# Performance work log

Hardware: AMD Instinct MI355X
Metric: run time of the kernel (lower is better)

Reference implementation:

```python
import jax, jax.numpy as jnp
import numpy as np

N = 100000   # nodes
E = 1600000  # edges
F = 128      # num_features
H = 128      # embedding_size
C = 10       # num_classes
G = 64       # graphs in batch


def setup_inputs() -> dict:
    key = jax.random.key(0)
    ks = jax.random.split(key, 10)
    x = jax.random.normal(ks[0], (N, F), jnp.float32)
    edge_index = jax.random.randint(ks[1], (2, E), 0, N)
    batch_index = jnp.sort(jax.random.randint(ks[2], (N,), 0, G))
    glorot = lambda k, shape: jax.random.normal(k, shape, jnp.float32) / np.float32(np.sqrt(shape[0]))
    return {
        "x": x, "edge_index": edge_index, "batch_index": batch_index,
        "W0": glorot(ks[3], (F, H)), "b0": jnp.zeros((H,), jnp.float32),
        "W1": glorot(ks[4], (H, H)), "b1": jnp.zeros((H,), jnp.float32),
        "W2": glorot(ks[5], (H, H)), "b2": jnp.zeros((H,), jnp.float32),
        "W3": glorot(ks[6], (H, H)), "b3": jnp.zeros((H,), jnp.float32),
        "Wout": glorot(ks[7], (2 * H, C)), "bout": jnp.zeros((C,), jnp.float32),
    }


def gcn_conv(x, W, b, src, dst):
    """PyG GCNConv: self-loops + symmetric D^-1/2 (A+I) D^-1/2 normalization."""
    n = x.shape[0]
    # degree with self-loop: deg[i] = 1 + in-degree(i)
    deg = 1.0 + jax.ops.segment_sum(jnp.ones(dst.shape[0], x.dtype), dst, num_segments=n)
    dinv = jax.lax.rsqrt(deg)
    h = x @ W  # [N, H]
    norm = (dinv[src] * dinv[dst])[:, None]  # [E, 1]
    agg = jax.ops.segment_sum(h[src] * norm, dst, num_segments=n)  # scatter-add over edges
    agg = agg + h * (1.0 / deg)[:, None]  # self-loop contribution dinv[i]^2 * h[i]
    return agg + b


def reference(x, edge_index, batch_index, W0, b0, W1, b1, W2, b2, W3, b3, Wout, bout):
    src, dst = edge_index[0], edge_index[1]
    h = jnp.tanh(gcn_conv(x, W0, b0, src, dst))
    h = jnp.tanh(gcn_conv(h, W1, b1, src, dst))
    h = jnp.tanh(gcn_conv(h, W2, b2, src, dst))
    h = jnp.tanh(gcn_conv(h, W3, b3, src, dst))
    # global max pool + global mean pool over batch_index
    gmax = jax.ops.segment_max(h, batch_index, num_segments=G)
    cnt = jax.ops.segment_sum(jnp.ones((h.shape[0],), h.dtype), batch_index, num_segments=G)
    gmean = jax.ops.segment_sum(h, batch_index, num_segments=G) / jnp.maximum(cnt, 1.0)[:, None]
    pooled = jnp.concatenate([gmax, gmean], axis=1)  # [G, 2H]
    out = pooled @ Wout + bout  # [G, C]
    return out, pooled
```

## Files before the change

### kernel.cpp

```cpp
#include <hip/hip_runtime.h>
#include <hip/hip_fp16.h>
#include <cmath>

typedef __attribute__((ext_vector_type(8))) short short8;
typedef __attribute__((ext_vector_type(8))) unsigned short ushort8;
typedef __attribute__((ext_vector_type(4))) float f32x4;

struct h8 { __half2 a, b, c, d; };

__device__ __forceinline__ unsigned pk_bf16(float a, float b) {
  unsigned r;
  asm("v_cvt_pk_bf16_f32 %0, %1, %2" : "=v"(r) : "v"(a), "v"(b));
  return r;
}

__device__ __forceinline__ float fast_tanh(float x) {
  float e2 = __expf(2.0f * x);
  return 1.0f - 2.0f * __builtin_amdgcn_rcpf(e2 + 1.0f);
}


__global__ __launch_bounds__(256) void count_k(const int* __restrict__ dst,
                                               int* __restrict__ cnt,
                                               int* __restrict__ epos, int E) {
  int e = blockIdx.x * 256 + threadIdx.x;
  if (e < E) epos[e] = atomicAdd(&cnt[dst[e]], 1);
}

__global__ __launch_bounds__(512) void scan_a(const int* __restrict__ cnt,
                                              int* __restrict__ rs,
                                              int* __restrict__ bsum,
                                              float* __restrict__ dinv,
                                              float* __restrict__ dinv2, int n) {
  __shared__ int s[512];
  int tid = threadIdx.x;
  int gid = blockIdx.x * 512 + tid;
  int v = (gid < n) ? cnt[gid] : 0;
  if (gid < n) {
    float deg = 1.0f + (float)v;
    dinv[gid] = rsqrtf(deg);
    dinv2[gid] = __builtin_amdgcn_rcpf(deg);
  }
  s[tid] = v;
  __syncthreads();
  for (int off = 1; off < 512; off <<= 1) {
    int t = (tid >= off) ? s[tid - off] : 0;
    __syncthreads();
    s[tid] += t;
    __syncthreads();
  }
  if (gid < n) rs[gid] = s[tid] - v;
  if (tid == 511) bsum[blockIdx.x] = s[511];
}

__global__ __launch_bounds__(256) void scan_b(const int* __restrict__ bsum,
                                              int* __restrict__ boff, int nb,
                                              const int* __restrict__ batch,
                                              int* __restrict__ gstart, int n,
                                              int G) {
  __shared__ int s[256];
  int tid = threadIdx.x;
  int v = (tid < nb) ? bsum[tid] : 0;
  s[tid] = v;
  __syncthreads();
  for (int off = 1; off < 256; off <<= 1) {
    int t = (tid >= off) ? s[tid - off] : 0;
    __syncthreads();
    s[tid] += t;
    __syncthreads();
  }
  if (tid < nb) boff[tid] = s[tid] - v;
  if (tid <= G) {
    int lo = 0, hi = n;
    while (lo < hi) {
      int mid = (lo + hi) >> 1;
      if (batch[mid] < tid) lo = mid + 1;
      else hi = mid;
    }
    gstart[tid] = lo;
  }
}

__global__ __launch_bounds__(512) void scan_c(const int* __restrict__ boff,
                                              int* __restrict__ rs, int n, int E) {
  int gid = blockIdx.x * 512 + threadIdx.x;
  if (gid < n) rs[gid] += boff[blockIdx.x];
  if (gid == 0) rs[n] = E;
}

__global__ __launch_bounds__(256) void fill_k(const int* __restrict__ src,
                                              const int* __restrict__ dst,
                                              const int* __restrict__ rs,
                                              const int* __restrict__ epos,
                                              const float* __restrict__ dinv,
                                              int2* __restrict__ edata, int E) {
  int e = blockIdx.x * 256 + threadIdx.x;
  if (e >= E) return;
  int s = src[e], d = dst[e];
  int pos = rs[d] + epos[e];
  int2 ed;
  ed.x = s;
  ed.y = __float_as_int(dinv[s] * dinv[d]);
  edata[pos] = ed;
}


__global__ __launch_bounds__(256) void wconv_all(const float* __restrict__ W0,
                                                 const float* __restrict__ W1,
                                                 const float* __restrict__ W2,
                                                 const float* __restrict__ W3,
                                                 unsigned short* __restrict__ WtHi,
                                                 unsigned short* __restrict__ WtLo) {
  int l = blockIdx.y;
  const float* W = (l == 0) ? W0 : (l == 1) ? W1 : (l == 2) ? W2 : W3;
  int idx = blockIdx.x * 256 + threadIdx.x;
  if (idx >= 8192) return;
  int n = idx & 127, k = (idx >> 7) * 2;
  float w0 = W[k * 128 + n], w1 = W[(k + 1) * 128 + n];
  unsigned h01 = pk_bf16(w0, w1);
  float hf0 = __uint_as_float(h01 << 16);
  float hf1 = __uint_as_float(h01 & 0xFFFF0000u);
  unsigned l01 = pk_bf16(w0 - hf0, w1 - hf1);
  *(unsigned*)&WtHi[l * 16384 + n * 128 + k] = h01;
  *(unsigned*)&WtLo[l * 16384 + n * 128 + k] = l01;
}


#define LDK 136

__global__ __launch_bounds__(256) void gemm_mfma(const float* __restrict__ A,
                                                 const unsigned short* __restrict__ WtHi,
                                                 const unsigned short* __restrict__ WtLo,
                                                 __half* __restrict__ O, int M) {
  __shared__ unsigned short sHi[128 * LDK];
  __shared__ unsigned short sLo[128 * LDK];
  int tid = threadIdx.x;
#pragma unroll
  for (int i = 0; i < 8; ++i) {
    int c = tid + i * 256;
    int n = c >> 4;
    int off = (c & 15) * 8;
    *(ushort8*)&sHi[n * LDK + off] = *(const ushort8*)&WtHi[c * 8];
    *(ushort8*)&sLo[n * LDK + off] = *(const ushort8*)&WtLo[c * 8];
  }
  __syncthreads();

  int wv = tid >> 6, lane = tid & 63;
  int r0 = blockIdx.x * 128 + wv * 32;
  int lrow = lane & 15, lk = (lane >> 4) * 8;

  f32x4 acc[2][8] = {};
#pragma unroll
  for (int kk = 0; kk < 4; ++kk) {
    int k0 = kk * 32 + lk;
    short8 ahi[2], alo[2];
#pragma unroll
    for (int fr = 0; fr < 2; ++fr) {
      int row = r0 + fr * 16 + lrow;
      row = row < M ? row : M - 1;
      const float* ap = &A[(size_t)row * 128 + k0];
      float4 a0 = *(const float4*)ap;
      float4 a1 = *(const float4*)(ap + 4);
      union { short8 v; unsigned u32[4]; } h_, l_;
#define SPLIT2(slot, x, y)                              \
      {                                                 \
        unsigned hh = pk_bf16((x), (y));                \
        h_.u32[slot] = hh;                              \
        float hf0 = __uint_as_float(hh << 16);          \
        float hf1 = __uint_as_float(hh & 0xFFFF0000u);  \
        l_.u32[slot] = pk_bf16((x) - hf0, (y) - hf1);   \
      }
      SPLIT2(0, a0.x, a0.y)
      SPLIT2(1, a0.z, a0.w)
      SPLIT2(2, a1.x, a1.y)
      SPLIT2(3, a1.z, a1.w)
#undef SPLIT2
      ahi[fr] = h_.v;
      alo[fr] = l_.v;
    }
#pragma unroll
    for (int c = 0; c < 8; ++c) {
      int bidx = (c * 16 + lrow) * LDK + k0;
      short8 bhi = *(const short8*)&sHi[bidx];
      short8 blo = *(const short8*)&sLo[bidx];
#pragma unroll
      for (int fr = 0; fr < 2; ++fr) {
        acc[fr][c] = __builtin_amdgcn_mfma_f32_16x16x32_bf16(ahi[fr], bhi, acc[fr][c], 0, 0, 0);
        acc[fr][c] = __builtin_amdgcn_mfma_f32_16x16x32_bf16(ahi[fr], blo, acc[fr][c], 0, 0, 0);
        acc[fr][c] = __builtin_amdgcn_mfma_f32_16x16x32_bf16(alo[fr], bhi, acc[fr][c], 0, 0, 0);
      }
    }
  }
#pragma unroll
  for (int fr = 0; fr < 2; ++fr) {
#pragma unroll
    for (int c = 0; c < 8; ++c) {
#pragma unroll
      for (int r = 0; r < 4; ++r) {
        int row = r0 + fr * 16 + (lane >> 4) * 4 + r;
        if (row < M)
          O[(size_t)row * 128 + c * 16 + (lane & 15)] = __float2half(acc[fr][c][r]);
      }
    }
  }
}

__global__ __launch_bounds__(256) void gemm_fast(const unsigned short* __restrict__ AHi,
                                                 const unsigned short* __restrict__ ALo,
                                                 const unsigned short* __restrict__ WtHi,
                                                 const unsigned short* __restrict__ WtLo,
                                                 __half* __restrict__ O, int M) {
  __shared__ unsigned short sHi[128 * LDK];
  __shared__ unsigned short sLo[128 * LDK];
  int tid = threadIdx.x;
#pragma unroll
  for (int i = 0; i < 8; ++i) {
    int c = tid + i * 256;
    int n = c >> 4;
    int off = (c & 15) * 8;
    *(ushort8*)&sHi[n * LDK + off] = *(const ushort8*)&WtHi[c * 8];
    *(ushort8*)&sLo[n * LDK + off] = *(const ushort8*)&WtLo[c * 8];
  }
  __syncthreads();

  int wv = tid >> 6, lane = tid & 63;
  int r0 = blockIdx.x * 128 + wv * 32;
  int lrow = lane & 15, lk = (lane >> 4) * 8;

  f32x4 acc[2][8] = {};
#pragma unroll
  for (int kk = 0; kk < 4; ++kk) {
    int k0 = kk * 32 + lk;
    short8 ahi[2], alo[2];
#pragma unroll
    for (int fr = 0; fr < 2; ++fr) {
      int row = r0 + fr * 16 + lrow;
      row = row < M ? row : M - 1;
      ahi[fr] = *(const short8*)&AHi[(size_t)row * 128 + k0];
      alo[fr] = *(const short8*)&ALo[(size_t)row * 128 + k0];
    }
#pragma unroll
    for (int c = 0; c < 8; ++c) {
      int bidx = (c * 16 + lrow) * LDK + k0;
      short8 bhi = *(const short8*)&sHi[bidx];
      short8 blo = *(const short8*)&sLo[bidx];
#pragma unroll
      for (int fr = 0; fr < 2; ++fr) {
        acc[fr][c] = __builtin_amdgcn_mfma_f32_16x16x32_bf16(ahi[fr], bhi, acc[fr][c], 0, 0, 0);
        acc[fr][c] = __builtin_amdgcn_mfma_f32_16x16x32_bf16(ahi[fr], blo, acc[fr][c], 0, 0, 0);
        acc[fr][c] = __builtin_amdgcn_mfma_f32_16x16x32_bf16(alo[fr], bhi, acc[fr][c], 0, 0, 0);
      }
    }
  }
#pragma unroll
  for (int fr = 0; fr < 2; ++fr) {
#pragma unroll
    for (int c = 0; c < 8; ++c) {
#pragma unroll
      for (int r = 0; r < 4; ++r) {
        int row = r0 + fr * 16 + (lane >> 4) * 4 + r;
        if (row < M)
          O[(size_t)row * 128 + c * 16 + (lane & 15)] = __float2half(acc[fr][c][r]);
      }
    }
  }
}


__global__ __launch_bounds__(256) void gather_k(const __half* __restrict__ h,
                                                const int* __restrict__ rs,
                                                const int2* __restrict__ edata,
                                                const float* __restrict__ dinv2,
                                                const float* __restrict__ bias,
                                                unsigned* __restrict__ OHi,
                                                unsigned* __restrict__ OLo, int N) {
  int wid = (int)((blockIdx.x * (size_t)blockDim.x + threadIdx.x) >> 6);
  if (wid >= N) return;
  int lane = threadIdx.x & 63;
  int grp = lane >> 4;
  int li = lane & 15;
  int s = rs[wid], e = rs[wid + 1];
  const h8* hrow = (const h8*)h;

  float ac[8] = {};
  int n16 = (e - s) >> 4;
  int base = s + grp;
  for (int it = 0; it < n16; ++it, base += 16) {
    int2 e0 = edata[base], e1 = edata[base + 4], e2 = edata[base + 8],
         e3 = edata[base + 12];
    float w0 = __int_as_float(e0.y), w1 = __int_as_float(e1.y),
          w2 = __int_as_float(e2.y), w3 = __int_as_float(e3.y);
    h8 v0 = hrow[(size_t)e0.x * 16 + li];
    h8 v1 = hrow[(size_t)e1.x * 16 + li];
    h8 v2 = hrow[(size_t)e2.x * 16 + li];
    h8 v3 = hrow[(size_t)e3.x * 16 + li];
#define ACC(V, W)                                    \
    {                                                \
      float2 f0 = __half22float2((V).a);             \
      float2 f1 = __half22float2((V).b);             \
      float2 f2 = __half22float2((V).c);             \
      float2 f3 = __half22float2((V).d);             \
      ac[0] += (W) * f0.x; ac[1] += (W) * f0.y;      \
      ac[2] += (W) * f1.x; ac[3] += (W) * f1.y;      \
      ac[4] += (W) * f2.x; ac[5] += (W) * f2.y;      \
      ac[6] += (W) * f3.x; ac[7] += (W) * f3.y;      \
    }
    ACC(v0, w0) ACC(v1, w1) ACC(v2, w2) ACC(v3, w3)
  }
  for (int idx = base; idx < e; idx += 4) {
    int2 ed = edata[idx];
    float w = __int_as_float(ed.y);
    h8 v = hrow[(size_t)ed.x * 16 + li];
    ACC(v, w)
  }
#undef ACC
#pragma unroll
  for (int j = 0; j < 8; ++j) {
    ac[j] += __shfl_xor(ac[j], 16);
    ac[j] += __shfl_xor(ac[j], 32);
  }

  float a0 = grp == 0 ? ac[0] : grp == 1 ? ac[2] : grp == 2 ? ac[4] : ac[6];
  float a1 = grp == 0 ? ac[1] : grp == 1 ? ac[3] : grp == 2 ? ac[5] : ac[7];

  float d2 = dinv2[wid];
  h8 sv = hrow[(size_t)wid * 16 + li];
  __half2 svh = grp == 0 ? sv.a : grp == 1 ? sv.b : grp == 2 ? sv.c : sv.d;
  float2 sj = __half22float2(svh);
  float2 bj = *(const float2*)&bias[li * 8 + 2 * grp];
  float o0 = fast_tanh(a0 + sj.x * d2 + bj.x);
  float o1 = fast_tanh(a1 + sj.y * d2 + bj.y);

  unsigned hp = pk_bf16(o0, o1);
  float r0f = __uint_as_float(hp << 16);
  float r1f = __uint_as_float(hp & 0xFFFF0000u);
  unsigned lp = pk_bf16(o0 - r0f, o1 - r1f);
  unsigned idx = (unsigned)wid * 64 + li * 4 + grp;
  OHi[idx] = hp;
  OLo[idx] = lp;
}


#define CH 16

__global__ __launch_bounds__(128) void pool_partial(const unsigned short* __restrict__ Hi,
                                                    const unsigned short* __restrict__ Lo,
                                                    const int* __restrict__ gstart,
                                                    float* __restrict__ pmax,
                                                    float* __restrict__ psum) {
  int g = blockIdx.x, c = blockIdx.y, f = threadIdx.x;
  int s = gstart[g], e = gstart[g + 1];
  long long len = e - s;
  int cs = s + (int)(len * c / CH);
  int ce = s + (int)(len * (c + 1) / CH);
  float m = -INFINITY, sum = 0.f;
  for (int n = cs; n < ce; ++n) {
    unsigned hv = Hi[(size_t)n * 128 + f];
    unsigned lv = Lo[(size_t)n * 128 + f];
    float v = __uint_as_float(hv << 16) + __uint_as_float(lv << 16);
    m = fmaxf(m, v);
    sum += v;
  }
  pmax[((size_t)g * CH + c) * 128 + f] = m;
  psum[((size_t)g * CH + c) * 128 + f] = sum;
}

__global__ __launch_bounds__(128) void pool_head(const float* __restrict__ pmax,
                                                 const float* __restrict__ psum,
                                                 const int* __restrict__ gstart,
                                                 const float* __restrict__ Wout,
                                                 const float* __restrict__ bout,
                                                 float* __restrict__ out, int G) {
  __shared__ float pl[256];
  int g = blockIdx.x, f = threadIdx.x;
  float m = -INFINITY, s = 0.f;
  for (int c = 0; c < CH; ++c) {
    m = fmaxf(m, pmax[((size_t)g * CH + c) * 128 + f]);
    s += psum[((size_t)g * CH + c) * 128 + f];
  }
  int cnt = gstart[g + 1] - gstart[g];
  float mean = s / fmaxf((float)cnt, 1.0f);
  float* pooled = out + (size_t)G * 10;
  pooled[(size_t)g * 256 + f] = m;
  pooled[(size_t)g * 256 + 128 + f] = mean;
  pl[f] = m;
  pl[128 + f] = mean;
  __syncthreads();
  if (f < 10) {
    float acc = bout[f];
    for (int k = 0; k < 256; ++k) acc += pl[k] * Wout[k * 10 + f];
    out[(size_t)g * 10 + f] = acc;
  }
}


extern "C" void kernel_launch(void* const* d_in, const int* in_sizes, int n_in,
                              void* d_out, int out_size, void* d_ws, size_t ws_size,
                              hipStream_t stream) {
  const float* x = (const float*)d_in[0];
  const int* ei = (const int*)d_in[1];
  const int* batch = (const int*)d_in[2];
  const float* W[4] = {(const float*)d_in[3], (const float*)d_in[5],
                       (const float*)d_in[7], (const float*)d_in[9]};
  const float* Bz[4] = {(const float*)d_in[4], (const float*)d_in[6],
                        (const float*)d_in[8], (const float*)d_in[10]};
  const float* Wout = (const float*)d_in[11];
  const float* bout = (const float*)d_in[12];
  const int N = in_sizes[0] / 128;
  const int E = in_sizes[1] / 2;
  const int G = 64;
  const int* srcp = ei;
  const int* dstp = ei + E;
  float* out = (float*)d_out;

  char* wsb = (char*)d_ws;
  size_t off = 0;
  auto alloc = [&](size_t bytes) -> void* {
    void* p = wsb + off;
    off = (off + bytes + 255) & ~(size_t)255;
    return p;
  };
  __half* bufA = (__half*)alloc((size_t)N * 128 * 2);
  unsigned* OHi = (unsigned*)alloc((size_t)N * 64 * 4);
  unsigned* OLo = (unsigned*)alloc((size_t)N * 64 * 4);
  int* cnt = (int*)alloc((size_t)N * 4);
  int* epos = (int*)alloc((size_t)E * 4);
  float* dinv = (float*)alloc((size_t)N * 4);
  float* dinv2 = (float*)alloc((size_t)N * 4);
  int* rs = (int*)alloc((size_t)(N + 1) * 4);
  int2* edata = (int2*)alloc((size_t)E * 8);
  int* bsum = (int*)alloc(4096);
  int* boff = (int*)alloc(4096);
  int* gstart = (int*)alloc(4096);
  float* pmax = (float*)alloc((size_t)G * CH * 128 * 4);
  float* psum = (float*)alloc((size_t)G * CH * 128 * 4);
  unsigned short* WtHi = (unsigned short*)alloc(4 * 16384 * 2);
  unsigned short* WtLo = (unsigned short*)alloc(4 * 16384 * 2);
  if (off > ws_size) return;

  hipMemsetAsync(cnt, 0, (size_t)N * 4, stream);

  count_k<<<(E + 255) / 256, 256, 0, stream>>>(dstp, cnt, epos, E);
  int nsb = (N + 511) / 512;
  scan_a<<<nsb, 512, 0, stream>>>(cnt, rs, bsum, dinv, dinv2, N);
  scan_b<<<1, 256, 0, stream>>>(bsum, boff, nsb, batch, gstart, N, G);
  scan_c<<<nsb, 512, 0, stream>>>(boff, rs, N, E);
  fill_k<<<(E + 255) / 256, 256, 0, stream>>>(srcp, dstp, rs, epos, dinv, edata, E);
  wconv_all<<<dim3(32, 4), 256, 0, stream>>>(W[0], W[1], W[2], W[3], WtHi, WtLo);

  for (int l = 0; l < 4; ++l) {
    if (l == 0)
      gemm_mfma<<<(N + 127) / 128, 256, 0, stream>>>(x, WtHi, WtLo, bufA, N);
    else
      gemm_fast<<<(N + 127) / 128, 256, 0, stream>>>((const unsigned short*)OHi,
                                                     (const unsigned short*)OLo,
                                                     WtHi + l * 16384,
                                                     WtLo + l * 16384, bufA, N);
    gather_k<<<((size_t)N * 64 + 255) / 256, 256, 0, stream>>>(bufA, rs, edata,
                                                               dinv2, Bz[l], OHi,
                                                               OLo, N);
  }

  pool_partial<<<dim3(G, CH), 128, 0, stream>>>((const unsigned short*)OHi,
                                                (const unsigned short*)OLo, gstart,
                                                pmax, psum);
  pool_head<<<G, 128, 0, stream>>>(pmax, psum, gstart, Wout, bout, out, G);
}
```

Before: 537.2 us.

## Store intermediate activations in fp16 and use split-fp16 weight MFMA for layers 1-3

The gather kernel now writes intermediate-layer activations as a single fp16 array instead of bf16 hi/lo pairs, which halves the bytes written and read between layers. Layers 1-3 use a new fp16 MFMA GEMM in which the weights are split into an fp16 high part and a residual scaled by 1024. This cuts the MFMA count from three to two per tile. The gather inner loop uses v_fma_mix_f32 to multiply fp16 values directly without explicit conversion. The cost is lower activation precision (fp16 in place of about 16-bit-mantissa bf16 pairs), and only the final layer keeps the hi/lo output for pooling.

```diff
diff --git a/kernel.cpp b/kernel.cpp
--- a/kernel.cpp
+++ b/kernel.cpp
@@ -4,9 +4,8 @@
 
 typedef __attribute__((ext_vector_type(8))) short short8;
 typedef __attribute__((ext_vector_type(8))) unsigned short ushort8;
+typedef __attribute__((ext_vector_type(8))) _Float16 f16x8;
 typedef __attribute__((ext_vector_type(4))) float f32x4;
-
-struct h8 { __half2 a, b, c, d; };
 
 __device__ __forceinline__ unsigned pk_bf16(float a, float b) {
   unsigned r;
@@ -18,6 +17,11 @@
   float e2 = __expf(2.0f * x);
   return 1.0f - 2.0f * __builtin_amdgcn_rcpf(e2 + 1.0f);
 }
+
+#define FM_LO(A, U, W) \
+  asm("v_fma_mix_f32 %0, %1, %2, %0 op_sel_hi:[1,0,0]" : "+v"(A) : "v"(U), "v"(W))
+#define FM_HI(A, U, W) \
+  asm("v_fma_mix_f32 %0, %1, %2, %0 op_sel:[1,0,0] op_sel_hi:[1,0,0]" : "+v"(A) : "v"(U), "v"(W))
 
 
 __global__ __launch_bounds__(256) void count_k(const int* __restrict__ dst,
@@ -109,20 +113,31 @@
                                                  const float* __restrict__ W1,
                                                  const float* __restrict__ W2,
                                                  const float* __restrict__ W3,
-                                                 unsigned short* __restrict__ WtHi,
-                                                 unsigned short* __restrict__ WtLo) {
+                                                 unsigned short* __restrict__ Wt0Hi,
+                                                 unsigned short* __restrict__ Wt0Lo,
+                                                 unsigned short* __restrict__ WfHi,
+                                                 unsigned short* __restrict__ WfLo) {
   int l = blockIdx.y;
   const float* W = (l == 0) ? W0 : (l == 1) ? W1 : (l == 2) ? W2 : W3;
   int idx = blockIdx.x * 256 + threadIdx.x;
   if (idx >= 8192) return;
   int n = idx & 127, k = (idx >> 7) * 2;
   float w0 = W[k * 128 + n], w1 = W[(k + 1) * 128 + n];
-  unsigned h01 = pk_bf16(w0, w1);
-  float hf0 = __uint_as_float(h01 << 16);
-  float hf1 = __uint_as_float(h01 & 0xFFFF0000u);
-  unsigned l01 = pk_bf16(w0 - hf0, w1 - hf1);
-  *(unsigned*)&WtHi[l * 16384 + n * 128 + k] = h01;
-  *(unsigned*)&WtLo[l * 16384 + n * 128 + k] = l01;
+  if (l == 0) {
+    unsigned h01 = pk_bf16(w0, w1);
+    float hf0 = __uint_as_float(h01 << 16);
+    float hf1 = __uint_as_float(h01 & 0xFFFF0000u);
+    unsigned l01 = pk_bf16(w0 - hf0, w1 - hf1);
+    *(unsigned*)&Wt0Hi[n * 128 + k] = h01;
+    *(unsigned*)&Wt0Lo[n * 128 + k] = l01;
+  } else {
+    __half2 hh = __float22half2_rn(make_float2(w0, w1));
+    float r0 = __low2float(hh), r1 = __high2float(hh);
+    __half2 ll = __float22half2_rn(make_float2((w0 - r0) * 1024.0f,
+                                               (w1 - r1) * 1024.0f));
+    *(__half2*)&WfHi[(l - 1) * 16384 + n * 128 + k] = hh;
+    *(__half2*)&WfLo[(l - 1) * 16384 + n * 128 + k] = ll;
+  }
 }
 
 
@@ -205,11 +220,11 @@
   }
 }
 
-__global__ __launch_bounds__(256) void gemm_fast(const unsigned short* __restrict__ AHi,
-                                                 const unsigned short* __restrict__ ALo,
-                                                 const unsigned short* __restrict__ WtHi,
-                                                 const unsigned short* __restrict__ WtLo,
-                                                 __half* __restrict__ O, int M) {
+
+__global__ __launch_bounds__(256) void gemm_f16(const __half* __restrict__ Hf,
+                                                const unsigned short* __restrict__ Whi,
+                                                const unsigned short* __restrict__ Wlo,
+                                                __half* __restrict__ O, int M) {
   __shared__ unsigned short sHi[128 * LDK];
   __shared__ unsigned short sLo[128 * LDK];
   int tid = threadIdx.x;
@@ -218,8 +233,8 @@
     int c = tid + i * 256;
     int n = c >> 4;
     int off = (c & 15) * 8;
-    *(ushort8*)&sHi[n * LDK + off] = *(const ushort8*)&WtHi[c * 8];
-    *(ushort8*)&sLo[n * LDK + off] = *(const ushort8*)&WtLo[c * 8];
+    *(ushort8*)&sHi[n * LDK + off] = *(const ushort8*)&Whi[c * 8];
+    *(ushort8*)&sLo[n * LDK + off] = *(const ushort8*)&Wlo[c * 8];
   }
   __syncthreads();
 
@@ -228,30 +243,30 @@
   int lrow = lane & 15, lk = (lane >> 4) * 8;
 
   f32x4 acc[2][8] = {};
+  f32x4 accL[2][8] = {};
 #pragma unroll
   for (int kk = 0; kk < 4; ++kk) {
     int k0 = kk * 32 + lk;
-    short8 ahi[2], alo[2];
+    f16x8 a[2];
 #pragma unroll
     for (int fr = 0; fr < 2; ++fr) {
       int row = r0 + fr * 16 + lrow;
       row = row < M ? row : M - 1;
-      ahi[fr] = *(const short8*)&AHi[(size_t)row * 128 + k0];
-      alo[fr] = *(const short8*)&ALo[(size_t)row * 128 + k0];
+      a[fr] = *(const f16x8*)&Hf[(size_t)row * 128 + k0];
     }
 #pragma unroll
     for (int c = 0; c < 8; ++c) {
       int bidx = (c * 16 + lrow) * LDK + k0;
-      short8 bhi = *(const short8*)&sHi[bidx];
-      short8 blo = *(const short8*)&sLo[bidx];
+      f16x8 bhi = *(const f16x8*)&sHi[bidx];
+      f16x8 blo = *(const f16x8*)&sLo[bidx];
 #pragma unroll
       for (int fr = 0; fr < 2; ++fr) {
-        acc[fr][c] = __builtin_amdgcn_mfma_f32_16x16x32_bf16(ahi[fr], bhi, acc[fr][c], 0, 0, 0);
-        acc[fr][c] = __builtin_amdgcn_mfma_f32_16x16x32_bf16(ahi[fr], blo, acc[fr][c], 0, 0, 0);
-        acc[fr][c] = __builtin_amdgcn_mfma_f32_16x16x32_bf16(alo[fr], bhi, acc[fr][c], 0, 0, 0);
+        acc[fr][c] = __builtin_amdgcn_mfma_f32_16x16x32_f16(a[fr], bhi, acc[fr][c], 0, 0, 0);
+        accL[fr][c] = __builtin_amdgcn_mfma_f32_16x16x32_f16(a[fr], blo, accL[fr][c], 0, 0, 0);
       }
     }
   }
+  const float ls = 1.0f / 1024.0f;
 #pragma unroll
   for (int fr = 0; fr < 2; ++fr) {
 #pragma unroll
@@ -260,18 +275,21 @@
       for (int r = 0; r < 4; ++r) {
         int row = r0 + fr * 16 + (lane >> 4) * 4 + r;
         if (row < M)
-          O[(size_t)row * 128 + c * 16 + (lane & 15)] = __float2half(acc[fr][c][r]);
+          O[(size_t)row * 128 + c * 16 + (lane & 15)] =
+              __float2half(acc[fr][c][r] + accL[fr][c][r] * ls);
       }
     }
   }
 }
 
 
+template <bool FINAL>
 __global__ __launch_bounds__(256) void gather_k(const __half* __restrict__ h,
                                                 const int* __restrict__ rs,
                                                 const int2* __restrict__ edata,
                                                 const float* __restrict__ dinv2,
                                                 const float* __restrict__ bias,
+                                                __half* __restrict__ Hf,
                                                 unsigned* __restrict__ OHi,
                                                 unsigned* __restrict__ OLo, int N) {
   int wid = (int)((blockIdx.x * (size_t)blockDim.x + threadIdx.x) >> 6);
@@ -280,37 +298,33 @@
   int grp = lane >> 4;
   int li = lane & 15;
   int s = rs[wid], e = rs[wid + 1];
-  const h8* hrow = (const h8*)h;
+  const uint4* hrow = (const uint4*)h;
 
   float ac[8] = {};
   int n16 = (e - s) >> 4;
   int base = s + grp;
+#define ACC(U, W)                                        \
+  {                                                      \
+    FM_LO(ac[0], (U).x, (W)); FM_HI(ac[1], (U).x, (W));  \
+    FM_LO(ac[2], (U).y, (W)); FM_HI(ac[3], (U).y, (W));  \
+    FM_LO(ac[4], (U).z, (W)); FM_HI(ac[5], (U).z, (W));  \
+    FM_LO(ac[6], (U).w, (W)); FM_HI(ac[7], (U).w, (W));  \
+  }
   for (int it = 0; it < n16; ++it, base += 16) {
     int2 e0 = edata[base], e1 = edata[base + 4], e2 = edata[base + 8],
          e3 = edata[base + 12];
     float w0 = __int_as_float(e0.y), w1 = __int_as_float(e1.y),
           w2 = __int_as_float(e2.y), w3 = __int_as_float(e3.y);
-    h8 v0 = hrow[(size_t)e0.x * 16 + li];
-    h8 v1 = hrow[(size_t)e1.x * 16 + li];
-    h8 v2 = hrow[(size_t)e2.x * 16 + li];
-    h8 v3 = hrow[(size_t)e3.x * 16 + li];
-#define ACC(V, W)                                    \
-    {                                                \
-      float2 f0 = __half22float2((V).a);             \
-      float2 f1 = __half22float2((V).b);             \
-      float2 f2 = __half22float2((V).c);             \
-      float2 f3 = __half22float2((V).d);             \
-      ac[0] += (W) * f0.x; ac[1] += (W) * f0.y;      \
-      ac[2] += (W) * f1.x; ac[3] += (W) * f1.y;      \
-      ac[4] += (W) * f2.x; ac[5] += (W) * f2.y;      \
-      ac[6] += (W) * f3.x; ac[7] += (W) * f3.y;      \
-    }
+    uint4 v0 = hrow[(size_t)e0.x * 16 + li];
+    uint4 v1 = hrow[(size_t)e1.x * 16 + li];
+    uint4 v2 = hrow[(size_t)e2.x * 16 + li];
+    uint4 v3 = hrow[(size_t)e3.x * 16 + li];
     ACC(v0, w0) ACC(v1, w1) ACC(v2, w2) ACC(v3, w3)
   }
   for (int idx = base; idx < e; idx += 4) {
     int2 ed = edata[idx];
     float w = __int_as_float(ed.y);
-    h8 v = hrow[(size_t)ed.x * 16 + li];
+    uint4 v = hrow[(size_t)ed.x * 16 + li];
     ACC(v, w)
   }
 #undef ACC
@@ -324,20 +338,25 @@
   float a1 = grp == 0 ? ac[1] : grp == 1 ? ac[3] : grp == 2 ? ac[5] : ac[7];
 
   float d2 = dinv2[wid];
-  h8 sv = hrow[(size_t)wid * 16 + li];
-  __half2 svh = grp == 0 ? sv.a : grp == 1 ? sv.b : grp == 2 ? sv.c : sv.d;
-  float2 sj = __half22float2(svh);
+  uint4 sv = hrow[(size_t)wid * 16 + li];
+  unsigned su = grp == 0 ? sv.x : grp == 1 ? sv.y : grp == 2 ? sv.z : sv.w;
+  float2 sj = __half22float2(*(__half2*)&su);
   float2 bj = *(const float2*)&bias[li * 8 + 2 * grp];
   float o0 = fast_tanh(a0 + sj.x * d2 + bj.x);
   float o1 = fast_tanh(a1 + sj.y * d2 + bj.y);
 
-  unsigned hp = pk_bf16(o0, o1);
-  float r0f = __uint_as_float(hp << 16);
-  float r1f = __uint_as_float(hp & 0xFFFF0000u);
-  unsigned lp = pk_bf16(o0 - r0f, o1 - r1f);
-  unsigned idx = (unsigned)wid * 64 + li * 4 + grp;
-  OHi[idx] = hp;
-  OLo[idx] = lp;
+  if (FINAL) {
+    unsigned hp = pk_bf16(o0, o1);
+    float r0f = __uint_as_float(hp << 16);
+    float r1f = __uint_as_float(hp & 0xFFFF0000u);
+    unsigned lp = pk_bf16(o0 - r0f, o1 - r1f);
+    unsigned idx = (unsigned)wid * 64 + li * 4 + grp;
+    OHi[idx] = hp;
+    OLo[idx] = lp;
+  } else {
+    __half2 hv = __float22half2_rn(make_float2(o0, o1));
+    *(__half2*)&Hf[(size_t)wid * 128 + li * 8 + 2 * grp] = hv;
+  }
 }
 
 
@@ -421,6 +440,7 @@
     return p;
   };
   __half* bufA = (__half*)alloc((size_t)N * 128 * 2);
+  __half* Hf = (__half*)alloc((size_t)N * 128 * 2);
   unsigned* OHi = (unsigned*)alloc((size_t)N * 64 * 4);
   unsigned* OLo = (unsigned*)alloc((size_t)N * 64 * 4);
   int* cnt = (int*)alloc((size_t)N * 4);
@@ -434,8 +454,10 @@
   int* gstart = (int*)alloc(4096);
   float* pmax = (float*)alloc((size_t)G * CH * 128 * 4);
   float* psum = (float*)alloc((size_t)G * CH * 128 * 4);
-  unsigned short* WtHi = (unsigned short*)alloc(4 * 16384 * 2);
-  unsigned short* WtLo = (unsigned short*)alloc(4 * 16384 * 2);
+  unsigned short* Wt0Hi = (unsigned short*)alloc(16384 * 2);
+  unsigned short* Wt0Lo = (unsigned short*)alloc(16384 * 2);
+  unsigned short* WfHi = (unsigned short*)alloc(3 * 16384 * 2);
+  unsigned short* WfLo = (unsigned short*)alloc(3 * 16384 * 2);
   if (off > ws_size) return;
 
   hipMemsetAsync(cnt, 0, (size_t)N * 4, stream);
@@ -446,19 +468,22 @@
   scan_b<<<1, 256, 0, stream>>>(bsum, boff, nsb, batch, gstart, N, G);
   scan_c<<<nsb, 512, 0, stream>>>(boff, rs, N, E);
   fill_k<<<(E + 255) / 256, 256, 0, stream>>>(srcp, dstp, rs, epos, dinv, edata, E);
-  wconv_all<<<dim3(32, 4), 256, 0, stream>>>(W[0], W[1], W[2], W[3], WtHi, WtLo);
-
+  wconv_all<<<dim3(32, 4), 256, 0, stream>>>(W[0], W[1], W[2], W[3], Wt0Hi, Wt0Lo,
+                                             WfHi, WfLo);
+
+  int ggrid = (int)(((size_t)N * 64 + 255) / 256);
   for (int l = 0; l < 4; ++l) {
     if (l == 0)
-      gemm_mfma<<<(N + 127) / 128, 256, 0, stream>>>(x, WtHi, WtLo, bufA, N);
+      gemm_mfma<<<(N + 127) / 128, 256, 0, stream>>>(x, Wt0Hi, Wt0Lo, bufA, N);
     else
-      gemm_fast<<<(N + 127) / 128, 256, 0, stream>>>((const unsigned short*)OHi,
-                                                     (const unsigned short*)OLo,
-                                                     WtHi + l * 16384,
-                                                     WtLo + l * 16384, bufA, N);
-    gather_k<<<((size_t)N * 64 + 255) / 256, 256, 0, stream>>>(bufA, rs, edata,
-                                                               dinv2, Bz[l], OHi,
-                                                               OLo, N);
+      gemm_f16<<<(N + 127) / 128, 256, 0, stream>>>(Hf, WfHi + (l - 1) * 16384,
+                                                    WfLo + (l - 1) * 16384, bufA, N);
+    if (l < 3)
+      gather_k<false><<<ggrid, 256, 0, stream>>>(bufA, rs, edata, dinv2, Bz[l], Hf,
+                                                 OHi, OLo, N);
+    else
+      gather_k<true><<<ggrid, 256, 0, stream>>>(bufA, rs, edata, dinv2, Bz[l], Hf,
+                                                OHi, OLo, N);
   }
 
   pool_partial<<<dim3(G, CH), 128, 0, stream>>>((const unsigned short*)OHi,
```

New measurement: 526.6 us. 1.02x faster.
